# Optimization experiments

Hardware: AMD Instinct MI355X
Metric: run time of the kernel (lower is better)

The kernel has to match this reference:

```python
import jax, jax.numpy as jnp
import numpy as np

RES = 100          # resolution
ITERS = 1000       # lowfid solver iterations
INIT_MIN = 0.01    # conductivity floor (init_min)
BATCH = 32
HIDDEN = [128, 256, 512]


def conductivity_original(pores, res):
    """Coarse 5x5 pore map -> base conductivity on the fine res x res grid.
    pore present (1) -> low conductivity (0), solid (0) -> conductivity 1."""
    B = pores.shape[0]
    grid = 1.0 - pores.reshape(B, 5, 5)
    f = res // 5
    return jnp.repeat(jnp.repeat(grid, f, axis=1), f, axis=2)  # (B, res, res)


def mlp_forward(x, params):
    n = len(params)
    for i, (W, b) in enumerate(params):
        x = x @ W + b
        if i < n - 1:
            x = jax.nn.relu(x)
    return x


def lowfid_solve(k):
    """1000-iteration Jacobi relaxation of variable-coefficient steady heat
    equation with T=1 on top edge, T=0 on bottom edge, insulated sides.
    Returns effective conductivity kappa per sample, shape (B,)."""
    B, res, _ = k.shape
    # face conductivities (arithmetic mean of adjacent cells, edge-padded)
    kp = jnp.pad(k, ((0, 0), (1, 1), (1, 1)), mode='edge')
    kN = 0.5 * (k + kp[:, :-2, 1:-1])
    kS = 0.5 * (k + kp[:, 2:, 1:-1])
    kW = 0.5 * (k + kp[:, 1:-1, :-2])
    kE = 0.5 * (k + kp[:, 1:-1, 2:])
    denom = kN + kS + kW + kE + 1e-12

    def step(T, _):
        Tp = jnp.pad(T, ((0, 0), (0, 0), (1, 1)), mode='edge')        # side Neumann
        Tp = jnp.pad(Tp, ((0, 0), (1, 1), (0, 0)))                    # top/bottom Dirichlet
        Tp = Tp.at[:, 0, :].set(1.0)                                   # T=1 at top, T=0 at bottom
        T_new = (kN * Tp[:, :-2, 1:-1] + kS * Tp[:, 2:, 1:-1]
                 + kW * Tp[:, 1:-1, :-2] + kE * Tp[:, 1:-1, 2:]) / denom
        return T_new, None

    T0 = jnp.broadcast_to(jnp.linspace(1.0, 0.0, res)[None, :, None], (B, res, res))
    T, _ = jax.lax.scan(step, T0, None, length=ITERS)
    # heat flux through top boundary; domain size 1, dT = 1 -> kappa = mean flux
    kappa = jnp.mean(2.0 * res * k[:, 0, :] * (1.0 - T[:, 0, :]), axis=1)
    return kappa


def setup_inputs() -> dict:
    key = jax.random.key(0)
    ks = jax.random.split(key, 10)
    pores = (jax.random.uniform(ks[0], (BATCH, 25)) > 0.5).astype(jnp.float32)
    sizes = [25] + HIDDEN + [RES * RES]
    inp = {"pores": pores}
    for i in range(len(sizes) - 1):
        fan_in = sizes[i]
        W = jax.random.normal(ks[1 + 2 * i], (sizes[i], sizes[i + 1]), jnp.float32) * np.sqrt(2.0 / fan_in)
        b = jnp.zeros((sizes[i + 1],), jnp.float32)
        inp[f"W{i + 1}"] = W
        inp[f"b{i + 1}"] = b
    return inp


def reference(pores, W1, b1, W2, b2, W3, b3, W4, b4):
    params = [(W1, b1), (W2, b2), (W3, b3), (W4, b4)]
    B = pores.shape[0]
    gen = mlp_forward(pores.reshape(B, 25), params).reshape(B, RES, RES)
    cond = gen + conductivity_original(pores, RES)   # learn_residual
    cond = jnp.maximum(cond, INIT_MIN)               # relu clamp to init_min
    kappa = lowfid_solve(cond)
    return kappa, cond
```

## Files before the change

kernel.cpp:

```cpp
#include <hip/hip_runtime.h>
#include <hip/hip_bf16.h>

#define RES   100
#define ITERS 1000
#define SLOTP 128

typedef float vf2 __attribute__((ext_vector_type(2)));

__global__ __launch_bounds__(256) void mlp123(const float* __restrict__ pores,
                                              const float* __restrict__ W1, const float* __restrict__ b1,
                                              const float* __restrict__ W2, const float* __restrict__ b2,
                                              const float* __restrict__ W3, const float* __restrict__ b3,
                                              float* __restrict__ x3out) {
    __shared__ float x1[128];
    __shared__ float x2[256];
    const int s = blockIdx.x, tid = threadIdx.x;

    if (tid < 128) {
        float acc = b1[tid];
#pragma unroll
        for (int k = 0; k < 25; ++k)
            acc = fmaf(pores[s * 25 + k], W1[k * 128 + tid], acc);
        x1[tid] = fmaxf(acc, 0.0f);
    }
    __syncthreads();

    {
        float acc = b2[tid];
#pragma unroll 8
        for (int k = 0; k < 128; ++k)
            acc = fmaf(x1[k], W2[k * 256 + tid], acc);
        x2[tid] = fmaxf(acc, 0.0f);
    }
    __syncthreads();

    {
        float a0 = b3[tid], a1 = b3[tid + 256];
#pragma unroll 8
        for (int k = 0; k < 256; ++k) {
            float xv = x2[k];
            a0 = fmaf(xv, W3[k * 512 + tid],       a0);
            a1 = fmaf(xv, W3[k * 512 + tid + 256], a1);
        }
        x3out[s * 512 + tid]       = fmaxf(a0, 0.0f);
        x3out[s * 512 + tid + 256] = fmaxf(a1, 0.0f);
    }
}

__global__ __launch_bounds__(256) void fc4_fused(const float* __restrict__ X3,
                                                 const float* __restrict__ W4,
                                                 const float* __restrict__ b4,
                                                 const float* __restrict__ pores,
                                                 float* __restrict__ cond) {
    const int j = blockIdx.x * 256 + threadIdx.x;
    if (j >= RES * RES) return;
    const int bg = blockIdx.y;
    const float* x = X3 + bg * 8 * 512;

    float acc[8];
    float bj = b4[j];
#pragma unroll
    for (int b = 0; b < 8; ++b) acc[b] = bj;

    for (int k0 = 0; k0 < 512; k0 += 8) {
        float w[8];
#pragma unroll
        for (int u = 0; u < 8; ++u)
            w[u] = W4[(k0 + u) * (RES * RES) + j];
#pragma unroll
        for (int u = 0; u < 8; ++u) {
#pragma unroll
            for (int b = 0; b < 8; ++b)
                acc[b] = fmaf(x[b * 512 + k0 + u], w[u], acc[b]);
        }
    }

    const int row = j / RES, col = j % RES;
    const int p = (row / 20) * 5 + (col / 20);
#pragma unroll
    for (int b = 0; b < 8; ++b) {
        int bb = bg * 8 + b;
        float base = 1.0f - pores[bb * 25 + p];
        cond[bb * RES * RES + j] = fmaxf(acc[b] + base, 0.01f);
    }
}

__device__ __forceinline__ float dpp_shr1(float old_v, float src) {
    return __int_as_float(__builtin_amdgcn_update_dpp(
        __float_as_int(old_v), __float_as_int(src), 0x138, 0xf, 0xf, false));
}
__device__ __forceinline__ float dpp_shl1(float old_v, float src) {
    return __int_as_float(__builtin_amdgcn_update_dpp(
        __float_as_int(old_v), __float_as_int(src), 0x130, 0xf, 0xf, false));
}

template<int R>
__device__ __forceinline__ void jstep(const vf2* __restrict__ nptr, const vf2* __restrict__ sptr,
                                      vf2* __restrict__ topptr, vf2* __restrict__ botptr,
                                      const vf2* wN, const vf2* wS,
                                      const vf2* wA, const vf2* wB,
                                      const vf2* Tin, vf2* Tout, bool fix49) {
    vf2 nval = *nptr;
    vf2 sval = *sptr;
#pragma unroll
    for (int r = 0; r < R; ++r) {
        vf2 nb = (r == 0)     ? nval : Tin[r - 1];
        vf2 sb = (r == R - 1) ? sval : Tin[r + 1];
        float lo = Tin[r].x, hi = Tin[r].y;
        float wlo = dpp_shr1(lo, hi);
        float ehi = dpp_shl1(hi, lo);
        ehi = fix49 ? hi : ehi;
        vf2 P1; P1.x = wlo; P1.y = ehi;
        vf2 TS; TS.x = hi;  TS.y = lo;
        Tout[r] = wN[r] * nb + wS[r] * sb + wA[r] * P1 + wB[r] * TS;
    }
    *topptr = Tout[0];
    *botptr = Tout[R - 1];
}

__global__ __launch_bounds__(1024) void jacobi(const float* __restrict__ cond,
                                               float* __restrict__ kappa_out) {
    __shared__ float kst[RES * RES];
    __shared__ float SA[34 * SLOTP];
    __shared__ float SB[34 * SLOTP];

    const int b   = blockIdx.x;
    const int tid = threadIdx.x;

    for (int i = tid; i < RES * RES; i += 1024)
        kst[i] = cond[b * RES * RES + i];
    if (tid < SLOTP) {
        SA[32 * SLOTP + tid] = 1.0f;  SA[33 * SLOTP + tid] = 0.0f;
        SB[32 * SLOTP + tid] = 1.0f;  SB[33 * SLOTP + tid] = 0.0f;
    }
    __syncthreads();

    const int w    = tid >> 6;
    const int lane = tid & 63;
    const int R    = (w < 4) ? 7 : 6;
    const int r0   = (w < 4) ? 7 * w : 28 + 6 * (w - 4);
    const int c0   = min(2 * lane, 98), c1 = c0 + 1;
    const int lane2 = 2 * lane;
    const bool fix49 = (lane == 49);

    vf2 wN[7], wS[7], wA[7], wB[7], T0[7], T1[7];

#pragma unroll
    for (int r = 0; r < 7; ++r) {
        if (r < R) {
            int i   = r0 + r;
            int in_ = i ? i - 1 : 0;
            int is_ = (i < RES - 1) ? i + 1 : RES - 1;
            int jw  = c0 ? c0 - 1 : 0;
            int je  = (c1 < RES - 1) ? c1 + 1 : RES - 1;
            float kc0 = kst[i * RES + c0], kc1 = kst[i * RES + c1];
            float kn0 = 0.5f * (kc0 + kst[in_ * RES + c0]);
            float kn1 = 0.5f * (kc1 + kst[in_ * RES + c1]);
            float ks0 = 0.5f * (kc0 + kst[is_ * RES + c0]);
            float ks1 = 0.5f * (kc1 + kst[is_ * RES + c1]);
            float kw0 = 0.5f * (kc0 + kst[i * RES + jw]);
            float kw1 = 0.5f * (kc1 + kc0);
            float ke0 = 0.5f * (kc0 + kc1);
            float ke1 = 0.5f * (kc1 + kst[i * RES + je]);
            float inv0 = 1.0f / (kn0 + ks0 + kw0 + ke0 + 1e-12f);
            float inv1 = 1.0f / (kn1 + ks1 + kw1 + ke1 + 1e-12f);
            wN[r].x = kn0 * inv0;  wN[r].y = kn1 * inv1;
            wS[r].x = ks0 * inv0;  wS[r].y = ks1 * inv1;
            wA[r].x = kw0 * inv0;  wA[r].y = ke1 * inv1;
            wB[r].x = ke0 * inv0;  wB[r].y = kw1 * inv1;
            float v = 1.0f - (float)i * (1.0f / (RES - 1));
            T0[r].x = v;  T0[r].y = v;
        }
    }

    vf2 bot0 = (w < 4) ? T0[6] : T0[5];
    *(vf2*)(SA + (2 * w) * SLOTP + lane2)     = T0[0];
    *(vf2*)(SA + (2 * w + 1) * SLOTP + lane2) = bot0;
    __syncthreads();

    const int nslot = (w == 0)  ? 32 : (2 * w - 1);
    const int sslot = (w == 15) ? 33 : (2 * w + 2);
    const int topsl = 2 * w;

    const vf2* SAn = (const vf2*)(SA + nslot * SLOTP + lane2);
    const vf2* SAs = (const vf2*)(SA + sslot * SLOTP + lane2);
    const vf2* SBn = (const vf2*)(SB + nslot * SLOTP + lane2);
    const vf2* SBs = (const vf2*)(SB + sslot * SLOTP + lane2);
    vf2* SAtop = (vf2*)(SA + topsl * SLOTP + lane2);
    vf2* SAbot = (vf2*)(SA + (topsl + 1) * SLOTP + lane2);
    vf2* SBtop = (vf2*)(SB + topsl * SLOTP + lane2);
    vf2* SBbot = (vf2*)(SB + (topsl + 1) * SLOTP + lane2);

    for (int it = 0; it < ITERS / 2; ++it) {
        if (w < 4) jstep<7>(SAn, SAs, SBtop, SBbot, wN, wS, wA, wB, T0, T1, fix49);
        else       jstep<6>(SAn, SAs, SBtop, SBbot, wN, wS, wA, wB, T0, T1, fix49);
        __syncthreads();
        if (w < 4) jstep<7>(SBn, SBs, SAtop, SAbot, wN, wS, wA, wB, T1, T0, fix49);
        else       jstep<6>(SBn, SBs, SAtop, SAbot, wN, wS, wA, wB, T1, T0, fix49);
        __syncthreads();
    }

    if (w == 0) {
        float s = 0.0f;
        if (lane < 50)
            s = kst[c0] * (1.0f - T0[0].x) + kst[c1] * (1.0f - T0[0].y);
        for (int off = 32; off; off >>= 1)
            s += __shfl_down(s, off);
        if (lane == 0) kappa_out[b] = 2.0f * s;
    }
}

extern "C" void kernel_launch(void* const* d_in, const int* in_sizes, int n_in,
                              void* d_out, int out_size, void* d_ws, size_t ws_size,
                              hipStream_t stream) {
    (void)in_sizes; (void)n_in; (void)out_size; (void)ws_size;
    const float* pores = (const float*)d_in[0];
    const float* W1 = (const float*)d_in[1];
    const float* b1 = (const float*)d_in[2];
    const float* W2 = (const float*)d_in[3];
    const float* b2 = (const float*)d_in[4];
    const float* W3 = (const float*)d_in[5];
    const float* b3 = (const float*)d_in[6];
    const float* W4 = (const float*)d_in[7];
    const float* b4 = (const float*)d_in[8];

    float* x3 = (float*)d_ws;

    float* kappa = (float*)d_out;
    float* cond  = kappa + 32;

    mlp123<<<32, 256, 0, stream>>>(pores, W1, b1, W2, b2, W3, b3, x3);
    fc4_fused<<<dim3(40, 4), 256, 0, stream>>>(x3, W4, b4, pores, cond);
    jacobi<<<32, 1024, 0, stream>>>(cond, kappa);
}
```

Baseline: 648.1 us.

## Replace block barriers in Jacobi loop with neighbor-wave LDS flag sync

The Jacobi solver no longer calls `__syncthreads` twice per iteration. Each wave now publishes a per-wave step counter in shared memory and spin-waits only on the flags of its north and south neighbor waves. The step also computes its interior rows first and the halo-dependent edge rows last, so the independent work can overlap the wait. This is meant to cut full-block barrier cost and let waves drift relative to each other, at the cost of LDS spin polling and a correctness burden around memory ordering of the halo exchange.

Result: slower. 685.2 us (+5.7%).

```diff
diff --git a/kernel.cpp b/kernel.cpp
--- a/kernel.cpp
+++ b/kernel.cpp
@@ -94,26 +94,40 @@
         __float_as_int(old_v), __float_as_int(src), 0x130, 0xf, 0xf, false));
 }
 
+__device__ __forceinline__ vf2 jrow(vf2 nb, vf2 sb, vf2 c,
+                                    vf2 wNr, vf2 wSr, vf2 wAr, vf2 wBr, bool fix49) {
+    float lo = c.x, hi = c.y;
+    float wlo = dpp_shr1(lo, hi);
+    float ehi = dpp_shl1(hi, lo);
+    ehi = fix49 ? hi : ehi;
+    vf2 P1; P1.x = wlo; P1.y = ehi;
+    vf2 TS; TS.x = hi;  TS.y = lo;
+    return wNr * nb + wSr * sb + wAr * P1 + wBr * TS;
+}
+
 template<int R>
-__device__ __forceinline__ void jstep(const vf2* __restrict__ nptr, const vf2* __restrict__ sptr,
-                                      vf2* __restrict__ topptr, vf2* __restrict__ botptr,
-                                      const vf2* wN, const vf2* wS,
-                                      const vf2* wA, const vf2* wB,
-                                      const vf2* Tin, vf2* Tout, bool fix49) {
+__device__ __forceinline__ void jstep2(const vf2* __restrict__ nptr, const vf2* __restrict__ sptr,
+                                       vf2* __restrict__ topptr, vf2* __restrict__ botptr,
+                                       const vf2* wN, const vf2* wS,
+                                       const vf2* wA, const vf2* wB,
+                                       const vf2* Tin, vf2* Tout, bool fix49,
+                                       volatile const int* flgN, volatile const int* flgS,
+                                       int swait) {
+#pragma unroll
+    for (int r = 1; r < R - 1; ++r)
+        Tout[r] = jrow(Tin[r - 1], Tin[r + 1], Tin[r], wN[r], wS[r], wA[r], wB[r], fix49);
+
+    if (flgN) { while (*flgN < swait) {} }
+    asm volatile("" ::: "memory");
     vf2 nval = *nptr;
+    if (flgS) { while (*flgS < swait) {} }
+    asm volatile("" ::: "memory");
     vf2 sval = *sptr;
-#pragma unroll
-    for (int r = 0; r < R; ++r) {
-        vf2 nb = (r == 0)     ? nval : Tin[r - 1];
-        vf2 sb = (r == R - 1) ? sval : Tin[r + 1];
-        float lo = Tin[r].x, hi = Tin[r].y;
-        float wlo = dpp_shr1(lo, hi);
-        float ehi = dpp_shl1(hi, lo);
-        ehi = fix49 ? hi : ehi;
-        vf2 P1; P1.x = wlo; P1.y = ehi;
-        vf2 TS; TS.x = hi;  TS.y = lo;
-        Tout[r] = wN[r] * nb + wS[r] * sb + wA[r] * P1 + wB[r] * TS;
-    }
+
+    Tout[0]     = jrow(nval, Tin[1], Tin[0], wN[0], wS[0], wA[0], wB[0], fix49);
+    Tout[R - 1] = jrow(Tin[R - 2], sval, Tin[R - 1],
+                       wN[R - 1], wS[R - 1], wA[R - 1], wB[R - 1], fix49);
+
     *topptr = Tout[0];
     *botptr = Tout[R - 1];
 }
@@ -123,6 +137,7 @@
     __shared__ float kst[RES * RES];
     __shared__ float SA[34 * SLOTP];
     __shared__ float SB[34 * SLOTP];
+    __shared__ int   flg[16];
 
     const int b   = blockIdx.x;
     const int tid = threadIdx.x;
@@ -133,6 +148,7 @@
         SA[32 * SLOTP + tid] = 1.0f;  SA[33 * SLOTP + tid] = 0.0f;
         SB[32 * SLOTP + tid] = 1.0f;  SB[33 * SLOTP + tid] = 0.0f;
     }
+    if (tid < 16) flg[tid] = -1;
     __syncthreads();
 
     const int w    = tid >> 6;
@@ -173,11 +189,6 @@
         }
     }
 
-    vf2 bot0 = (w < 4) ? T0[6] : T0[5];
-    *(vf2*)(SA + (2 * w) * SLOTP + lane2)     = T0[0];
-    *(vf2*)(SA + (2 * w + 1) * SLOTP + lane2) = bot0;
-    __syncthreads();
-
     const int nslot = (w == 0)  ? 32 : (2 * w - 1);
     const int sslot = (w == 15) ? 33 : (2 * w + 2);
     const int topsl = 2 * w;
@@ -191,13 +202,26 @@
     vf2* SBtop = (vf2*)(SB + topsl * SLOTP + lane2);
     vf2* SBbot = (vf2*)(SB + (topsl + 1) * SLOTP + lane2);
 
+    volatile const int* vfN = (w > 0)  ? (volatile const int*)&flg[w - 1] : (volatile const int*)0;
+    volatile const int* vfS = (w < 15) ? (volatile const int*)&flg[w + 1] : (volatile const int*)0;
+    volatile int*       vfMe = (volatile int*)&flg[w];
+
+    vf2 bot0 = (w < 4) ? T0[6] : T0[5];
+    *SAtop = T0[0];
+    *SAbot = bot0;
+    asm volatile("s_waitcnt lgkmcnt(0)" ::: "memory");
+    if (lane == 0) *vfMe = 0;
+
     for (int it = 0; it < ITERS / 2; ++it) {
-        if (w < 4) jstep<7>(SAn, SAs, SBtop, SBbot, wN, wS, wA, wB, T0, T1, fix49);
-        else       jstep<6>(SAn, SAs, SBtop, SBbot, wN, wS, wA, wB, T0, T1, fix49);
-        __syncthreads();
-        if (w < 4) jstep<7>(SBn, SBs, SAtop, SAbot, wN, wS, wA, wB, T1, T0, fix49);
-        else       jstep<6>(SBn, SBs, SAtop, SAbot, wN, wS, wA, wB, T1, T0, fix49);
-        __syncthreads();
+        const int s0 = 2 * it;
+        if (w < 4) jstep2<7>(SAn, SAs, SBtop, SBbot, wN, wS, wA, wB, T0, T1, fix49, vfN, vfS, s0);
+        else       jstep2<6>(SAn, SAs, SBtop, SBbot, wN, wS, wA, wB, T0, T1, fix49, vfN, vfS, s0);
+        asm volatile("s_waitcnt lgkmcnt(0)" ::: "memory");
+        if (lane == 0) *vfMe = s0 + 1;
+        if (w < 4) jstep2<7>(SBn, SBs, SAtop, SAbot, wN, wS, wA, wB, T1, T0, fix49, vfN, vfS, s0 + 1);
+        else       jstep2<6>(SBn, SBs, SAtop, SAbot, wN, wS, wA, wB, T1, T0, fix49, vfN, vfS, s0 + 1);
+        asm volatile("s_waitcnt lgkmcnt(0)" ::: "memory");
+        if (lane == 0) *vfMe = s0 + 2;
     }
 
     if (w == 0) {
```

## Split Jacobi solve across four blocks per sample with global-memory halo exchange

Applied to the files above, without the earlier changes.

Replaces the single 1024-thread block per sample with four 512-thread blocks, each owning 25 rows, so 128 workgroups run on more CUs. Each block redundantly computes 4 ghost rows on each side, which lets it exchange halos through global memory with flag-based spin waits only every 4 iterations instead of every step. This removes the per-sample CU bottleneck and shortens each block's per-iteration work. In exchange it adds redundant ghost-row compute, inter-block spin synchronisation that assumes all 128 blocks are co-resident, and an extra memset launch. The old single-block kernel is kept as a fallback when the workspace is too small.

After: 1.577 ms. +143.3%, slower.

```diff
diff --git a/kernel.cpp b/kernel.cpp
--- a/kernel.cpp
+++ b/kernel.cpp
@@ -4,8 +4,11 @@
 #define RES   100
 #define ITERS 1000
 #define SLOTP 128
+#define NGROUPS (ITERS / 4)
 
 typedef float vf2 __attribute__((ext_vector_type(2)));
+
+__device__ __forceinline__ vf2 mk2(float a, float b) { vf2 r; r.x = a; r.y = b; return r; }
 
 __global__ __launch_bounds__(256) void mlp123(const float* __restrict__ pores,
                                               const float* __restrict__ W1, const float* __restrict__ b1,
@@ -94,6 +97,33 @@
         __float_as_int(old_v), __float_as_int(src), 0x130, 0xf, 0xf, false));
 }
 
+__device__ __forceinline__ vf2 jrow(vf2 nb, vf2 sb, vf2 c,
+                                    vf2 wNr, vf2 wSr, vf2 wAr, vf2 wBr, bool fix49) {
+    float lo = c.x, hi = c.y;
+    float wlo = dpp_shr1(lo, hi);
+    float ehi = dpp_shl1(hi, lo);
+    ehi = fix49 ? hi : ehi;
+    vf2 P1; P1.x = wlo; P1.y = ehi;
+    vf2 TS; TS.x = hi;  TS.y = lo;
+    return wNr * nb + wSr * sb + wAr * P1 + wBr * TS;
+}
+
+template<int R>
+__device__ __forceinline__ void substepT(vf2 nin, vf2 sin,
+                                         const vf2* wN, const vf2* wS,
+                                         const vf2* wA, const vf2* wB,
+                                         const vf2* Tin, vf2* Tout, bool fix49,
+                                         vf2* topptr, vf2* botptr) {
+    Tout[0] = jrow(nin, Tin[1], Tin[0], wN[0], wS[0], wA[0], wB[0], fix49);
+#pragma unroll
+    for (int r = 1; r < R - 1; ++r)
+        Tout[r] = jrow(Tin[r - 1], Tin[r + 1], Tin[r], wN[r], wS[r], wA[r], wB[r], fix49);
+    Tout[R - 1] = jrow(Tin[R - 2], sin, Tin[R - 1],
+                       wN[R - 1], wS[R - 1], wA[R - 1], wB[R - 1], fix49);
+    *topptr = Tout[0];
+    *botptr = Tout[R - 1];
+}
+
 template<int R>
 __device__ __forceinline__ void jstep(const vf2* __restrict__ nptr, const vf2* __restrict__ sptr,
                                       vf2* __restrict__ topptr, vf2* __restrict__ botptr,
@@ -106,13 +136,7 @@
     for (int r = 0; r < R; ++r) {
         vf2 nb = (r == 0)     ? nval : Tin[r - 1];
         vf2 sb = (r == R - 1) ? sval : Tin[r + 1];
-        float lo = Tin[r].x, hi = Tin[r].y;
-        float wlo = dpp_shr1(lo, hi);
-        float ehi = dpp_shl1(hi, lo);
-        ehi = fix49 ? hi : ehi;
-        vf2 P1; P1.x = wlo; P1.y = ehi;
-        vf2 TS; TS.x = hi;  TS.y = lo;
-        Tout[r] = wN[r] * nb + wS[r] * sb + wA[r] * P1 + wB[r] * TS;
+        Tout[r] = jrow(nb, sb, Tin[r], wN[r], wS[r], wA[r], wB[r], fix49);
     }
     *topptr = Tout[0];
     *botptr = Tout[R - 1];
@@ -210,10 +234,188 @@
     }
 }
 
+__global__ __launch_bounds__(512) void jacobi4(const float* __restrict__ cond,
+                                               float* __restrict__ kappa_out,
+                                               float* __restrict__ haloDn,
+                                               float* __restrict__ haloUp,
+                                               int* __restrict__ flagDn,
+                                               int* __restrict__ flagUp) {
+    __shared__ float kst[35 * 100];
+    __shared__ float SA[16 * SLOTP];
+    __shared__ float SB[16 * SLOTP];
+
+    const int blk = blockIdx.x;
+    const int s   = blk & 31;
+    const int p   = blk >> 5;
+    const int tid = threadIdx.x;
+    const int R0  = 25 * p;
+    const int kLo = (p == 0) ? 0 : R0 - 5;
+    const int kHi = (p == 3) ? 99 : R0 + 29;
+    const int nk  = (kHi - kLo + 1) * 100;
+
+    for (int i = tid; i < nk; i += 512)
+        kst[i] = cond[s * RES * RES + kLo * 100 + i];
+    __syncthreads();
+
+    const int w    = tid >> 6;
+    const int lane = tid & 63;
+    const int R    = (w == 0 || w == 7) ? 4 : (w == 6 ? 2 : 3);
+    const int rb   = (w == 0) ? 0 : (w == 7) ? 21 : (w == 6) ? 19 : (1 + 3 * w);
+    const int c0   = min(2 * lane, 98), c1 = c0 + 1;
+    const int lane2 = 2 * lane;
+    const bool fix49 = (lane == 49);
+    const bool hasN = (w == 0 && p > 0);
+    const bool hasS = (w == 7 && p < 3);
+
+    auto kat = [&](int gi, int c) { return kst[(gi - kLo) * 100 + c]; };
+    auto mkw = [&](int gi, vf2& wn, vf2& ws_, vf2& wa, vf2& wb, vf2& t) {
+        int in_ = gi ? gi - 1 : 0;
+        int is_ = (gi < RES - 1) ? gi + 1 : RES - 1;
+        int jw  = c0 ? c0 - 1 : 0;
+        int je  = (c1 < RES - 1) ? c1 + 1 : RES - 1;
+        float kc0 = kat(gi, c0), kc1 = kat(gi, c1);
+        float kn0 = 0.5f * (kc0 + kat(in_, c0));
+        float kn1 = 0.5f * (kc1 + kat(in_, c1));
+        float ks0 = 0.5f * (kc0 + kat(is_, c0));
+        float ks1 = 0.5f * (kc1 + kat(is_, c1));
+        float kw0 = 0.5f * (kc0 + kat(gi, jw));
+        float kw1 = 0.5f * (kc1 + kc0);
+        float ke0 = 0.5f * (kc0 + kc1);
+        float ke1 = 0.5f * (kc1 + kat(gi, je));
+        float inv0 = 1.0f / (kn0 + ks0 + kw0 + ke0 + 1e-12f);
+        float inv1 = 1.0f / (kn1 + ks1 + kw1 + ke1 + 1e-12f);
+        wn  = mk2(kn0 * inv0, kn1 * inv1);
+        ws_ = mk2(ks0 * inv0, ks1 * inv1);
+        wa  = mk2(kw0 * inv0, ke1 * inv1);
+        wb  = mk2(ke0 * inv0, kw1 * inv1);
+        float v = 1.0f - (float)gi * (1.0f / (RES - 1));
+        t = mk2(v, v);
+    };
+
+    vf2 wN[4], wS[4], wA[4], wB[4], T0[4], T1[4];
+#pragma unroll
+    for (int r = 0; r < 4; ++r)
+        if (r < R) mkw(R0 + rb + r, wN[r], wS[r], wA[r], wB[r], T0[r]);
+
+    vf2 hwN[4], hwS[4], hwA[4], hwB[4], hA[4], hB[4];
+    vf2 gwN[4], gwS[4], gwA[4], gwB[4], gA[4], gB[4];
+    if (hasN) {
+#pragma unroll
+        for (int i = 0; i < 4; ++i)
+            mkw(R0 - 4 + i, hwN[i], hwS[i], hwA[i], hwB[i], hA[i]);
+    }
+    if (hasS) {
+#pragma unroll
+        for (int i = 0; i < 4; ++i)
+            mkw(R0 + 25 + i, gwN[i], gwS[i], gwA[i], gwB[i], gA[i]);
+    }
+
+    const int nsl = (w > 0) ? 2 * w - 1 : 0;
+    const int ssl = (w < 7) ? 2 * w + 2 : 0;
+    const vf2* AN = (const vf2*)(SA + nsl * SLOTP + lane2);
+    const vf2* AS = (const vf2*)(SA + ssl * SLOTP + lane2);
+    const vf2* BN = (const vf2*)(SB + nsl * SLOTP + lane2);
+    const vf2* BS = (const vf2*)(SB + ssl * SLOTP + lane2);
+    vf2* ATp = (vf2*)(SA + (2 * w) * SLOTP + lane2);
+    vf2* ABt = (vf2*)(SA + (2 * w + 1) * SLOTP + lane2);
+    vf2* BTp = (vf2*)(SB + (2 * w) * SLOTP + lane2);
+    vf2* BBt = (vf2*)(SB + (2 * w + 1) * SLOTP + lane2);
+
+    vf2 bot0 = (R == 4) ? T0[3] : (R == 3 ? T0[2] : T0[1]);
+    *ATp = T0[0];
+    *ABt = bot0;
+    __syncthreads();
+
+#define SUBX(TI, TO, NSL, SSL, TPL, BPL, HIN, HOUT, GIN, GOUT, SUB)                              \
+    {                                                                                            \
+        vf2 nin, sin;                                                                            \
+        if (w == 0) nin = (p == 0) ? mk2(1.0f, 1.0f) : HIN[3];                                   \
+        else        nin = *NSL;                                                                  \
+        if (w == 7) sin = (p == 3) ? mk2(0.0f, 0.0f) : GIN[0];                                   \
+        else        sin = *SSL;                                                                  \
+        if (hasN) {                                                                              \
+            if (SUB < 1) HOUT[1] = jrow(HIN[0], HIN[2], HIN[1], hwN[1], hwS[1], hwA[1], hwB[1], fix49); \
+            if (SUB < 2) HOUT[2] = jrow(HIN[1], HIN[3], HIN[2], hwN[2], hwS[2], hwA[2], hwB[2], fix49); \
+            if (SUB < 3) HOUT[3] = jrow(HIN[2], TI[0],  HIN[3], hwN[3], hwS[3], hwA[3], hwB[3], fix49); \
+        }                                                                                        \
+        if (hasS) {                                                                              \
+            if (SUB < 3) GOUT[0] = jrow(TI[3],  GIN[1], GIN[0], gwN[0], gwS[0], gwA[0], gwB[0], fix49); \
+            if (SUB < 2) GOUT[1] = jrow(GIN[0], GIN[2], GIN[1], gwN[1], gwS[1], gwA[1], gwB[1], fix49); \
+            if (SUB < 1) GOUT[2] = jrow(GIN[1], GIN[3], GIN[2], gwN[2], gwS[2], gwA[2], gwB[2], fix49); \
+        }                                                                                        \
+        if (w == 0 || w == 7) substepT<4>(nin, sin, wN, wS, wA, wB, TI, TO, fix49, TPL, BPL);    \
+        else if (w == 6)      substepT<2>(nin, sin, wN, wS, wA, wB, TI, TO, fix49, TPL, BPL);    \
+        else                  substepT<3>(nin, sin, wN, wS, wA, wB, TI, TO, fix49, TPL, BPL);    \
+        __syncthreads();                                                                         \
+    }
+
+    for (int v = 0; v < NGROUPS; ++v) {
+        if (v) {
+            if (hasN) {
+                int* f = flagDn + s * 3 + (p - 1);
+                if (lane == 0)
+                    while (__hip_atomic_load(f, __ATOMIC_RELAXED, __HIP_MEMORY_SCOPE_AGENT) < v) {}
+                __builtin_amdgcn_fence(__ATOMIC_ACQUIRE, "agent");
+                const float* buf = haloDn + (((s * 3 + (p - 1)) * 2) + (v & 1)) * 512;
+#pragma unroll
+                for (int i = 0; i < 4; ++i)
+                    hA[i] = *(const vf2*)(buf + i * 128 + lane2);
+            }
+            if (hasS) {
+                int* f = flagUp + s * 3 + p;
+                if (lane == 0)
+                    while (__hip_atomic_load(f, __ATOMIC_RELAXED, __HIP_MEMORY_SCOPE_AGENT) < v) {}
+                __builtin_amdgcn_fence(__ATOMIC_ACQUIRE, "agent");
+                const float* buf = haloUp + (((s * 3 + p) * 2) + (v & 1)) * 512;
+#pragma unroll
+                for (int i = 0; i < 4; ++i)
+                    gA[i] = *(const vf2*)(buf + i * 128 + lane2);
+            }
+        }
+
+        SUBX(T0, T1, AN, AS, BTp, BBt, hA, hB, gA, gB, 0)
+        SUBX(T1, T0, BN, BS, ATp, ABt, hB, hA, gB, gA, 1)
+        SUBX(T0, T1, AN, AS, BTp, BBt, hA, hB, gA, gB, 2)
+        SUBX(T1, T0, BN, BS, ATp, ABt, hB, hA, gB, gA, 3)
+
+        if (v + 1 < NGROUPS) {
+            const int par = (v + 1) & 1;
+            if (hasS) {
+                float* buf = haloDn + ((s * 3 + p) * 2 + par) * 512;
+#pragma unroll
+                for (int i = 0; i < 4; ++i)
+                    *(vf2*)(buf + i * 128 + lane2) = T0[i];
+                __builtin_amdgcn_fence(__ATOMIC_RELEASE, "agent");
+                if (lane == 0)
+                    __hip_atomic_store(flagDn + s * 3 + p, v + 1, __ATOMIC_RELAXED, __HIP_MEMORY_SCOPE_AGENT);
+            }
+            if (hasN) {
+                float* buf = haloUp + ((s * 3 + (p - 1)) * 2 + par) * 512;
+#pragma unroll
+                for (int i = 0; i < 4; ++i)
+                    *(vf2*)(buf + i * 128 + lane2) = T0[i];
+                __builtin_amdgcn_fence(__ATOMIC_RELEASE, "agent");
+                if (lane == 0)
+                    __hip_atomic_store(flagUp + s * 3 + (p - 1), v + 1, __ATOMIC_RELAXED, __HIP_MEMORY_SCOPE_AGENT);
+            }
+        }
+    }
+#undef SUBX
+
+    if (p == 0 && w == 0) {
+        float sm = 0.0f;
+        if (lane < 50)
+            sm = kst[c0] * (1.0f - T0[0].x) + kst[c1] * (1.0f - T0[0].y);
+        for (int off = 32; off; off >>= 1)
+            sm += __shfl_down(sm, off);
+        if (lane == 0) kappa_out[s] = 2.0f * sm;
+    }
+}
+
 extern "C" void kernel_launch(void* const* d_in, const int* in_sizes, int n_in,
                               void* d_out, int out_size, void* d_ws, size_t ws_size,
                               hipStream_t stream) {
-    (void)in_sizes; (void)n_in; (void)out_size; (void)ws_size;
+    (void)in_sizes; (void)n_in; (void)out_size;
     const float* pores = (const float*)d_in[0];
     const float* W1 = (const float*)d_in[1];
     const float* b1 = (const float*)d_in[2];
@@ -225,11 +427,24 @@
     const float* b4 = (const float*)d_in[8];
 
     float* x3 = (float*)d_ws;
+    float* haloDn = x3 + 32 * 512;
+    float* haloUp = haloDn + 32 * 3 * 2 * 4 * 128;
+    int*   flagDn = (int*)(haloUp + 32 * 3 * 2 * 4 * 128);
+    int*   flagUp = flagDn + 32 * 3;
 
     float* kappa = (float*)d_out;
     float* cond  = kappa + 32;
 
+    const size_t need = (size_t)(32 * 512 + 2 * 32 * 3 * 2 * 4 * 128) * sizeof(float)
+                      + (size_t)(32 * 3 * 2) * sizeof(int);
+
     mlp123<<<32, 256, 0, stream>>>(pores, W1, b1, W2, b2, W3, b3, x3);
     fc4_fused<<<dim3(40, 4), 256, 0, stream>>>(x3, W4, b4, pores, cond);
-    jacobi<<<32, 1024, 0, stream>>>(cond, kappa);
-}
+
+    if (ws_size >= need) {
+        hipMemsetAsync(flagDn, 0, 32 * 3 * 2 * sizeof(int), stream);
+        jacobi4<<<128, 512, 0, stream>>>(cond, kappa, haloDn, haloUp, flagDn, flagUp);
+    } else {
+        jacobi<<<32, 1024, 0, stream>>>(cond, kappa);
+    }
+}
```

## Transpose FC4 activations, widen per-thread batch tile, reorder Jacobi halo rows

Applied to the files above, without the earlier changes.

The MLP's third-layer output is now stored transposed (k-major, batch-minor), so the final FC layer reads wave-uniform activation vectors. Each thread accumulates 16 batch outputs instead of 8, with two waves covering columns and two covering batch halves, and the grid shrinks to 79 blocks. This is meant to raise W4 reuse and cut per-FMA activation loads. The Jacobi step computes interior rows first and boundary rows last, so the halo stores issue right before the barrier. The trade-off is fewer blocks for the FC layer and higher register pressure.

Measured after the change: 674.8 us. 1.04x slower.

```diff
diff --git a/kernel.cpp b/kernel.cpp
--- a/kernel.cpp
+++ b/kernel.cpp
@@ -11,7 +11,7 @@
                                               const float* __restrict__ W1, const float* __restrict__ b1,
                                               const float* __restrict__ W2, const float* __restrict__ b2,
                                               const float* __restrict__ W3, const float* __restrict__ b3,
-                                              float* __restrict__ x3out) {
+                                              float* __restrict__ x3t) {
     __shared__ float x1[128];
     __shared__ float x2[256];
     const int s = blockIdx.x, tid = threadIdx.x;
@@ -42,44 +42,49 @@
             a0 = fmaf(xv, W3[k * 512 + tid],       a0);
             a1 = fmaf(xv, W3[k * 512 + tid + 256], a1);
         }
-        x3out[s * 512 + tid]       = fmaxf(a0, 0.0f);
-        x3out[s * 512 + tid + 256] = fmaxf(a1, 0.0f);
-    }
-}
-
-__global__ __launch_bounds__(256) void fc4_fused(const float* __restrict__ X3,
+        x3t[tid * 32 + s]         = fmaxf(a0, 0.0f);
+        x3t[(tid + 256) * 32 + s] = fmaxf(a1, 0.0f);
+    }
+}
+
+__global__ __launch_bounds__(256) void fc4_fused(const float* __restrict__ X3T,
                                                  const float* __restrict__ W4,
                                                  const float* __restrict__ b4,
                                                  const float* __restrict__ pores,
                                                  float* __restrict__ cond) {
-    const int j = blockIdx.x * 256 + threadIdx.x;
+    const int w    = threadIdx.x >> 6;
+    const int lane = threadIdx.x & 63;
+    const int jsub = w & 1;
+    const int bh   = __builtin_amdgcn_readfirstlane(w >> 1);
+    const int j    = blockIdx.x * 128 + jsub * 64 + lane;
     if (j >= RES * RES) return;
-    const int bg = blockIdx.y;
-    const float* x = X3 + bg * 8 * 512;
-
-    float acc[8];
+    const int b0 = bh * 16;
+
+    float acc[16];
     float bj = b4[j];
 #pragma unroll
-    for (int b = 0; b < 8; ++b) acc[b] = bj;
-
-    for (int k0 = 0; k0 < 512; k0 += 8) {
-        float w[8];
-#pragma unroll
-        for (int u = 0; u < 8; ++u)
-            w[u] = W4[(k0 + u) * (RES * RES) + j];
-#pragma unroll
-        for (int u = 0; u < 8; ++u) {
-#pragma unroll
-            for (int b = 0; b < 8; ++b)
-                acc[b] = fmaf(x[b * 512 + k0 + u], w[u], acc[b]);
+    for (int b = 0; b < 16; ++b) acc[b] = bj;
+
+    const float* __restrict__ xt = X3T + b0;
+
+    for (int k0 = 0; k0 < 512; k0 += 16) {
+        float wv[16];
+#pragma unroll
+        for (int u = 0; u < 16; ++u)
+            wv[u] = W4[(k0 + u) * (RES * RES) + j];
+#pragma unroll
+        for (int u = 0; u < 16; ++u) {
+#pragma unroll
+            for (int b = 0; b < 16; ++b)
+                acc[b] = fmaf(wv[u], xt[(k0 + u) * 32 + b], acc[b]);
         }
     }
 
     const int row = j / RES, col = j % RES;
     const int p = (row / 20) * 5 + (col / 20);
 #pragma unroll
-    for (int b = 0; b < 8; ++b) {
-        int bb = bg * 8 + b;
+    for (int b = 0; b < 16; ++b) {
+        int bb = b0 + b;
         float base = 1.0f - pores[bb * 25 + p];
         cond[bb * RES * RES + j] = fmaxf(acc[b] + base, 0.01f);
     }
@@ -92,6 +97,17 @@
 __device__ __forceinline__ float dpp_shl1(float old_v, float src) {
     return __int_as_float(__builtin_amdgcn_update_dpp(
         __float_as_int(old_v), __float_as_int(src), 0x130, 0xf, 0xf, false));
+}
+
+__device__ __forceinline__ vf2 jrow(vf2 nb, vf2 sb, vf2 c,
+                                    vf2 wNr, vf2 wSr, vf2 wAr, vf2 wBr, bool fix49) {
+    float lo = c.x, hi = c.y;
+    float wlo = dpp_shr1(lo, hi);
+    float ehi = dpp_shl1(hi, lo);
+    ehi = fix49 ? hi : ehi;
+    vf2 P1; P1.x = wlo; P1.y = ehi;
+    vf2 TS; TS.x = hi;  TS.y = lo;
+    return wNr * nb + wSr * sb + wAr * P1 + wBr * TS;
 }
 
 template<int R>
@@ -103,18 +119,12 @@
     vf2 nval = *nptr;
     vf2 sval = *sptr;
 #pragma unroll
-    for (int r = 0; r < R; ++r) {
-        vf2 nb = (r == 0)     ? nval : Tin[r - 1];
-        vf2 sb = (r == R - 1) ? sval : Tin[r + 1];
-        float lo = Tin[r].x, hi = Tin[r].y;
-        float wlo = dpp_shr1(lo, hi);
-        float ehi = dpp_shl1(hi, lo);
-        ehi = fix49 ? hi : ehi;
-        vf2 P1; P1.x = wlo; P1.y = ehi;
-        vf2 TS; TS.x = hi;  TS.y = lo;
-        Tout[r] = wN[r] * nb + wS[r] * sb + wA[r] * P1 + wB[r] * TS;
-    }
+    for (int r = 1; r < R - 1; ++r)
+        Tout[r] = jrow(Tin[r - 1], Tin[r + 1], Tin[r], wN[r], wS[r], wA[r], wB[r], fix49);
+    Tout[0] = jrow(nval, Tin[1], Tin[0], wN[0], wS[0], wA[0], wB[0], fix49);
     *topptr = Tout[0];
+    Tout[R - 1] = jrow(Tin[R - 2], sval, Tin[R - 1],
+                       wN[R - 1], wS[R - 1], wA[R - 1], wB[R - 1], fix49);
     *botptr = Tout[R - 1];
 }
 
@@ -224,12 +234,12 @@
     const float* W4 = (const float*)d_in[7];
     const float* b4 = (const float*)d_in[8];
 
-    float* x3 = (float*)d_ws;
+    float* x3t = (float*)d_ws;
 
     float* kappa = (float*)d_out;
     float* cond  = kappa + 32;
 
-    mlp123<<<32, 256, 0, stream>>>(pores, W1, b1, W2, b2, W3, b3, x3);
-    fc4_fused<<<dim3(40, 4), 256, 0, stream>>>(x3, W4, b4, pores, cond);
+    mlp123<<<32, 256, 0, stream>>>(pores, W1, b1, W2, b2, W3, b3, x3t);
+    fc4_fused<<<79, 256, 0, stream>>>(x3t, W4, b4, pores, cond);
     jacobi<<<32, 1024, 0, stream>>>(cond, kappa);
 }
```
